# Performance work log

Hardware: AMD Instinct MI355X
Metric: run time of the kernel (lower is better)

Reference implementation:

```python
import jax, jax.numpy as jnp
import numpy as np

EPS = 1e-5
BLOCKS = 8

def _bn(x, g, b, m, v):
    # eval-mode BatchNorm1d over channel dim of [B, C, T]
    return g[:, None] * (x - m[:, None]) * jax.lax.rsqrt(v[:, None] + EPS) + b[:, None]

def _conv1x1(x, w):
    # x: [B, Cin, T], w: [Cout, Cin] -> [B, Cout, T]
    return jnp.einsum('bct,oc->bot', x, w)

def _dwconv(x, w, dil):
    # x: [B, C, T], w: [C, K] depthwise dilated conv, 'same' padding
    C, K = w.shape
    pad = dil * (K - 1) // 2
    return jax.lax.conv_general_dilated(
        x, w[:, None, :], window_strides=(1,), padding=[(pad, pad)],
        rhs_dilation=(dil,), dimension_numbers=('NCH', 'OIH', 'NCH'),
        feature_group_count=C)

def setup_inputs() -> dict:
    key = jax.random.key(0)
    ks = jax.random.split(key, 16)
    B, Cb, H, T, K = 16, 256, 512, 4096, 3
    d = {}
    d['x'] = jax.random.normal(ks[0], (B, Cb, T), jnp.float32)
    d['bn1_gamma'] = jax.random.uniform(ks[1], (BLOCKS, Cb), jnp.float32)
    d['bn1_beta'] = jax.random.normal(ks[2], (BLOCKS, Cb), jnp.float32)
    d['bn1_mean'] = jax.random.normal(ks[3], (BLOCKS, Cb), jnp.float32)
    d['bn1_var'] = jax.random.uniform(ks[4], (BLOCKS, Cb), jnp.float32)
    d['w1'] = jax.random.normal(ks[5], (BLOCKS, H, Cb), jnp.float32)
    d['bn2_gamma'] = jax.random.uniform(ks[6], (BLOCKS, H), jnp.float32)
    d['bn2_beta'] = jax.random.normal(ks[7], (BLOCKS, H), jnp.float32)
    d['bn2_mean'] = jax.random.normal(ks[8], (BLOCKS, H), jnp.float32)
    d['bn2_var'] = jax.random.uniform(ks[9], (BLOCKS, H), jnp.float32)
    d['dw_w'] = jax.random.normal(ks[10], (BLOCKS, H, K), jnp.float32)
    d['bn3_gamma'] = jax.random.uniform(ks[11], (BLOCKS, H), jnp.float32)
    d['bn3_beta'] = jax.random.normal(ks[12], (BLOCKS, H), jnp.float32)
    d['bn3_mean'] = jax.random.normal(ks[13], (BLOCKS, H), jnp.float32)
    d['bn3_var'] = jax.random.uniform(ks[14], (BLOCKS, H), jnp.float32)
    d['w2'] = jax.random.normal(ks[15], (BLOCKS, Cb, H), jnp.float32)
    return d

def reference(x, bn1_gamma, bn1_beta, bn1_mean, bn1_var, w1,
              bn2_gamma, bn2_beta, bn2_mean, bn2_var, dw_w,
              bn3_gamma, bn3_beta, bn3_mean, bn3_var, w2):
    sign = jnp.sign  # binary activation on inputs and weights
    resid = x
    for i in range(BLOCKS):
        dil = 2 ** i
        h = _bn(resid, bn1_gamma[i], bn1_beta[i], bn1_mean[i], bn1_var[i])
        h = _conv1x1(sign(h), sign(w1[i]))                 # 1x1, Cb -> H
        h = _bn(h, bn2_gamma[i], bn2_beta[i], bn2_mean[i], bn2_var[i])
        h = _dwconv(sign(h), sign(dw_w[i]), dil)           # depthwise dilated
        h = _bn(h, bn3_gamma[i], bn3_beta[i], bn3_mean[i], bn3_var[i])
        h = _conv1x1(sign(h), sign(w2[i]))                 # 1x1, H -> Cb
        resid = resid + h
    return resid
```

## Files before the change

### kernel.cpp

```cpp
#include <hip/hip_runtime.h>
#include <stdint.h>

namespace {
constexpr int Bn  = 16;
constexpr int Cc  = 256;
constexpr int Hn  = 512;
constexpr int Tn  = 4096;
constexpr int CWn = Cc / 32;
constexpr int HWn = Hn / 32;
constexpr int TWn = Tn / 32;
constexpr int TC  = 64;
constexpr float EPSf = 1e-5f;
}

__global__ __launch_bounds__(256) void setup_kernel(
    const float* __restrict__ bn1g, const float* __restrict__ bn1b,
    const float* __restrict__ bn1m, const float* __restrict__ bn1v,
    const float* __restrict__ w1,
    const float* __restrict__ bn2g, const float* __restrict__ bn2b,
    const float* __restrict__ bn2m, const float* __restrict__ bn2v,
    const float* __restrict__ dww,
    const float* __restrict__ bn3g, const float* __restrict__ bn3b,
    const float* __restrict__ bn3m, const float* __restrict__ bn3v,
    const float* __restrict__ w2,
    float* __restrict__ thr1, float* __restrict__ thr2, float* __restrict__ thr3,
    uint32_t* __restrict__ dws, uint32_t* __restrict__ W1p, uint32_t* __restrict__ W2p)
{
  const int idx = blockIdx.x * 256 + threadIdx.x;
  if (idx < 8 * Hn * CWn) {
    const int w = idx & (CWn - 1);
    const int h = idx >> 3;
    const float* src = w1 + (size_t)h * Cc + w * 32;
    uint32_t word = 0;
#pragma unroll
    for (int j = 0; j < 32; ++j) word |= (uint32_t)(src[j] > 0.f) << j;
    W1p[h * CWn + w] = word;
  } else {
    const int k = idx - 8 * Hn * CWn;
    const int w = k & (HWn - 1);
    const int c = k >> 4;
    const float* src = w2 + (size_t)c * Hn + w * 32;
    uint32_t word = 0;
#pragma unroll
    for (int j = 0; j < 32; ++j) word |= (uint32_t)(src[j] > 0.f) << j;
    W2p[c * HWn + w] = word;
  }
  if (idx < 8 * Cc)
    thr1[idx] = bn1m[idx] - bn1b[idx] * sqrtf(bn1v[idx] + EPSf) / bn1g[idx];
  if (idx < 8 * Hn) {
    thr2[idx] = bn2m[idx] - bn2b[idx] * sqrtf(bn2v[idx] + EPSf) / bn2g[idx];
    thr3[idx] = bn3m[idx] - bn3b[idx] * sqrtf(bn3v[idx] + EPSf) / bn3g[idx];
    uint32_t dw = 0;
    for (int k = 0; k < 3; ++k) dw |= (uint32_t)(dww[(size_t)idx * 3 + k] > 0.f) << k;
    dws[idx] = dw;
  }
}

__global__ __launch_bounds__(256) void k1_pack(
    const float* __restrict__ resid, const float* __restrict__ thr1,
    uint32_t* __restrict__ Xp)
{
  const int idx = blockIdx.x * 256 + threadIdx.x;
  const int t  = idx & (Tn - 1);
  const int cw = (idx >> 12) & (CWn - 1);
  const int b  = idx >> 15;
  const float* r = resid + ((size_t)(b * Cc + cw * 32)) * Tn + t;
  uint32_t word = 0;
#pragma unroll
  for (int j = 0; j < 32; ++j)
    word |= (uint32_t)(r[(size_t)j * Tn] > thr1[cw * 32 + j]) << j;
  Xp[((size_t)b * CWn + cw) * Tn + t] = word;
}

__global__ __launch_bounds__(256) void k2_gemm1(
    const uint32_t* __restrict__ Xp, const uint32_t* __restrict__ W1p,
    const float* __restrict__ thr2, uint32_t* __restrict__ Y)
{
  const int bid  = blockIdx.x;
  const int tblk = bid & 15;
  const int og   = (bid >> 4) & 63;
  const int b    = bid >> 10;
  const int t    = tblk * 256 + threadIdx.x;
  const int o    = og * 8;

  const uint32_t* xrow = Xp + (size_t)b * CWn * Tn + t;
  const uint32_t* wrow = W1p + o * CWn;
  int acc[8] = {0, 0, 0, 0, 0, 0, 0, 0};
#pragma unroll
  for (int w = 0; w < CWn; ++w) {
    const uint32_t xw = xrow[(size_t)w * Tn];
#pragma unroll
    for (int r = 0; r < 8; ++r)
      acc[r] += __popc(xw ^ wrow[r * CWn + w]);
  }
  const int lane = threadIdx.x & 63;
#pragma unroll
  for (int r = 0; r < 8; ++r) {
    const float v = (float)(Cc - 2 * acc[r]);
    const uint64_t m = __ballot(v > thr2[o + r]);
    if ((lane & 31) == 0)
      Y[((size_t)b * TWn + (t >> 5)) * Hn + o + r] = (uint32_t)(m >> lane);
  }
}

__global__ __launch_bounds__(512) void k_iter(
    const uint32_t* __restrict__ Yin, const uint32_t* __restrict__ dws,
    const float* __restrict__ thr3, const uint32_t* __restrict__ W2p,
    const float* __restrict__ rin, float* __restrict__ rout,
    const float* __restrict__ thr1n, const uint32_t* __restrict__ W1n,
    const float* __restrict__ thr2n, uint32_t* __restrict__ Yout,
    int dil, int do_next)
{
  __shared__ uint32_t Zlds[HWn * TC];
  __shared__ uint32_t Xlds[CWn * TC];

  const int chunk = blockIdx.x & (Tn / TC - 1);
  const int b     = blockIdx.x >> 6;
  const int lane  = threadIdx.x & 63;
  const int wid   = __builtin_amdgcn_readfirstlane(threadIdx.x >> 6);
  const int lh    = lane & 31;
  const int twL   = lane >> 5;
  const int tw0   = chunk * 2;

#pragma unroll
  for (int task = 0; task < 2; ++task) {
    const int hw = wid * 2 + task;
    const int tw = tw0 + twL;
    const int ch = hw * 32 + lh;

    const uint32_t* yb = Yin + (size_t)b * TWn * Hn + ch;
    const uint32_t ycur = yb[(size_t)tw * Hn];
    uint32_t yl, yr, Vl, Vr;
    if (dil >= 32) {
      const int dw = dil >> 5;
      const bool lok = tw >= dw, rok = tw + dw < TWn;
      yl = lok ? yb[(size_t)(tw - dw) * Hn] : 0u;
      yr = rok ? yb[(size_t)(tw + dw) * Hn] : 0u;
      Vl = lok ? ~0u : 0u;
      Vr = rok ? ~0u : 0u;
    } else {
      const uint32_t yp = (tw > 0) ? yb[(size_t)(tw - 1) * Hn] : 0u;
      const uint32_t yn = (tw < TWn - 1) ? yb[(size_t)(tw + 1) * Hn] : 0u;
      yl = (ycur << dil) | ((tw > 0) ? (yp >> (32 - dil)) : 0u);
      yr = (ycur >> dil) | ((tw < TWn - 1) ? (yn << (32 - dil)) : 0u);
      Vl = (tw == 0) ? (~0u << dil) : ~0u;
      Vr = (tw == TWn - 1) ? (~0u >> dil) : ~0u;
    }
    const uint32_t d = dws[ch];
    const uint32_t a  = ((d & 1u) ? yl : ~yl) & Vl;
    const uint32_t bb = (d & 2u) ? ycur : ~ycur;
    const uint32_t c  = ((d & 4u) ? yr : ~yr) & Vr;

    const float thr = thr3[ch];
    const float v3 = (thr + 3.f) * 0.5f;
    const float v2 = (thr + 2.f) * 0.5f;
    const int K3 = (int)(v3 >= 0.f) + (int)(v3 >= 1.f) + (int)(v3 >= 2.f) + (int)(v3 >= 3.f);
    const int K2 = (int)(v2 >= 0.f) + (int)(v2 >= 1.f) + (int)(v2 >= 2.f);

    const uint32_t g1 = a | bb | c;
    const uint32_t g2 = (a & bb) | (c & (a | bb));
    const uint32_t g3 = a & bb & c;
    const uint32_t full = (K3 == 0) ? ~0u : (K3 == 1) ? g1 : (K3 == 2) ? g2
                        : (K3 == 3) ? g3 : 0u;
    const uint32_t lm = (K2 == 0) ? ~0u : (K2 == 1) ? (bb | c) : (K2 == 2) ? (bb & c) : 0u;
    const uint32_t rm = (K2 == 0) ? ~0u : (K2 == 1) ? (a | bb) : (K2 == 2) ? (a & bb) : 0u;

    uint32_t w = (Vl & Vr & full) | (~Vl & lm) | (~Vr & rm);

#pragma unroll
    for (int s = 16; s; s >>= 1) {
      const uint32_t m = 0xFFFFFFFFu / ((1u << s) + 1u);
      const uint32_t o = __shfl_xor(w, s, 64);
      w = ((lane & s) == 0) ? ((w & m) | ((o & m) << s))
                            : ((w & ~m) | ((o & ~m) >> s));
    }
    Zlds[hw * TC + twL * 32 + lh] = w;
  }
  __syncthreads();

  {
    const int cw = wid;
    const int tl = lane;
    const int tg = chunk * TC + tl;

    uint32_t z[HWn];
#pragma unroll
    for (int w = 0; w < HWn; ++w) z[w] = Zlds[w * TC + tl];

    const uint32_t* wrow = W2p + (cw * 32) * HWn;
    const size_t base = ((size_t)(b * Cc + cw * 32)) * Tn + tg;
    const float* rp = rin + base;
    float* op = rout + base;
    uint32_t word = 0;
#pragma unroll 1
    for (int jo = 0; jo < 32; jo += 8) {
      float rv[8];
#pragma unroll
      for (int jj = 0; jj < 8; ++jj)
        rv[jj] = rp[(size_t)(jo + jj) * Tn];
#pragma unroll
      for (int jj = 0; jj < 8; ++jj) {
        const int j = jo + jj;
        int acc = 0;
#pragma unroll
        for (int w = 0; w < HWn; ++w) acc += __popc(z[w] ^ wrow[j * HWn + w]);
        const float ro = rv[jj] + (float)(Hn - 2 * acc);
        op[(size_t)j * Tn] = ro;
        word |= (uint32_t)(ro > thr1n[cw * 32 + j]) << j;
      }
    }
    Xlds[cw * TC + tl] = word;
  }
  __syncthreads();

  if (do_next) {
    const int t  = chunk * TC + lane;
    uint32_t x[CWn];
#pragma unroll
    for (int w = 0; w < CWn; ++w) x[w] = Xlds[w * TC + lane];

    uint32_t* yo = Yout + ((size_t)b * TWn + (t >> 5)) * Hn;
#pragma unroll 1
    for (int r = 0; r < 8; ++r) {
      const int o = wid * 64 + r * 8;
      const uint32_t* wrow = W1n + o * CWn;
      int acc[8] = {0, 0, 0, 0, 0, 0, 0, 0};
#pragma unroll
      for (int w = 0; w < CWn; ++w) {
        const uint32_t xw = x[w];
#pragma unroll
        for (int q = 0; q < 8; ++q)
          acc[q] += __popc(xw ^ wrow[q * CWn + w]);
      }
#pragma unroll
      for (int q = 0; q < 8; ++q) {
        const float v = (float)(Cc - 2 * acc[q]);
        const uint64_t m = __ballot(v > thr2n[o + q]);
        if ((lane & 31) == 0)
          yo[o + q] = (uint32_t)(m >> lane);
      }
    }
  }
}

extern "C" void kernel_launch(void* const* d_in, const int* in_sizes, int n_in,
                              void* d_out, int out_size, void* d_ws, size_t ws_size,
                              hipStream_t stream)
{
  const float* x     = (const float*)d_in[0];
  const float* bn1g  = (const float*)d_in[1];
  const float* bn1b  = (const float*)d_in[2];
  const float* bn1m  = (const float*)d_in[3];
  const float* bn1v  = (const float*)d_in[4];
  const float* w1    = (const float*)d_in[5];
  const float* bn2g  = (const float*)d_in[6];
  const float* bn2b  = (const float*)d_in[7];
  const float* bn2m  = (const float*)d_in[8];
  const float* bn2v  = (const float*)d_in[9];
  const float* dww   = (const float*)d_in[10];
  const float* bn3g  = (const float*)d_in[11];
  const float* bn3b  = (const float*)d_in[12];
  const float* bn3m  = (const float*)d_in[13];
  const float* bn3v  = (const float*)d_in[14];
  const float* w2    = (const float*)d_in[15];
  float* out = (float*)d_out;

  char* ws = (char*)d_ws;
  uint32_t* Xp  = (uint32_t*)(ws);
  uint32_t* Ya  = (uint32_t*)(ws + (2u  << 20));
  uint32_t* Yb  = (uint32_t*)(ws + (6u  << 20));
  uint32_t* W1p = (uint32_t*)(ws + (10u << 20));
  uint32_t* W2p = (uint32_t*)(ws + (10u << 20) + (128u << 10));
  float*    thr1 = (float*)(ws + (10u << 20) + (256u << 10));
  float*    thr2 = thr1 + 8 * Cc;
  float*    thr3 = thr2 + 8 * Hn;
  uint32_t* dws  = (uint32_t*)(thr3 + 8 * Hn);

  setup_kernel<<<256, 256, 0, stream>>>(bn1g, bn1b, bn1m, bn1v, w1,
                                        bn2g, bn2b, bn2m, bn2v, dww,
                                        bn3g, bn3b, bn3m, bn3v, w2,
                                        thr1, thr2, thr3, dws, W1p, W2p);

  k1_pack <<<2048,  256, 0, stream>>>(x, thr1, Xp);
  k2_gemm1<<<16384, 256, 0, stream>>>(Xp, W1p, thr2, Ya);

  for (int i = 0; i < 8; ++i) {
    const float* rin = (i == 0) ? x : out;
    const int inext = (i < 7) ? i + 1 : 7;
    const uint32_t* Yin  = (i & 1) ? Yb : Ya;
    uint32_t*       Yout = (i & 1) ? Ya : Yb;
    k_iter<<<1024, 512, 0, stream>>>(Yin, dws + i * Hn, thr3 + i * Hn,
                                     W2p + i * Cc * HWn, rin, out,
                                     thr1 + inext * Cc, W1p + inext * Hn * CWn,
                                     thr2 + inext * Hn, Yout,
                                     1 << i, (i < 7) ? 1 : 0);
  }
}
```

Measured before the change: 437.6 us.

## Compute next-block binary GEMM1 with int8 MFMA instead of XOR-popcount

Result: faster. 382.2 us (-12.7%).

```diff
diff --git a/kernel.cpp b/kernel.cpp
--- a/kernel.cpp
+++ b/kernel.cpp
@@ -12,6 +12,9 @@
 constexpr int TC  = 64;
 constexpr float EPSf = 1e-5f;
 }
+
+typedef __attribute__((ext_vector_type(4)))  int i32x4;
+typedef __attribute__((ext_vector_type(16))) int i32x16;
 
 __global__ __launch_bounds__(256) void setup_kernel(
     const float* __restrict__ bn1g, const float* __restrict__ bn1b,
@@ -24,7 +27,8 @@
     const float* __restrict__ bn3m, const float* __restrict__ bn3v,
     const float* __restrict__ w2,
     float* __restrict__ thr1, float* __restrict__ thr2, float* __restrict__ thr3,
-    uint32_t* __restrict__ dws, uint32_t* __restrict__ W1p, uint32_t* __restrict__ W2p)
+    uint32_t* __restrict__ dws, uint32_t* __restrict__ W1p, uint32_t* __restrict__ W2p,
+    uint8_t* __restrict__ W1u, int* __restrict__ Sw1, int* __restrict__ T2i)
 {
   const int idx = blockIdx.x * 256 + threadIdx.x;
   if (idx < 8 * Hn * CWn) {
@@ -35,6 +39,14 @@
 #pragma unroll
     for (int j = 0; j < 32; ++j) word |= (uint32_t)(src[j] > 0.f) << j;
     W1p[h * CWn + w] = word;
+    atomicAdd(&Sw1[h], (int)__popc(word));
+    uint32_t* dst = (uint32_t*)(W1u + (size_t)h * 256);
+#pragma unroll
+    for (int q = 0; q < 8; ++q) {
+      const uint32_t dw = (((word >> (4 * q)) & 0xFu) * 0x00204081u) & 0x01010101u;
+      const int off = (w * 32 + q * 4) ^ ((h & 15) << 4);
+      dst[off >> 2] = dw;
+    }
   } else {
     const int k = idx - 8 * Hn * CWn;
     const int w = k & (HWn - 1);
@@ -48,10 +60,17 @@
   if (idx < 8 * Cc)
     thr1[idx] = bn1m[idx] - bn1b[idx] * sqrtf(bn1v[idx] + EPSf) / bn1g[idx];
   if (idx < 8 * Hn) {
-    thr2[idx] = bn2m[idx] - bn2b[idx] * sqrtf(bn2v[idx] + EPSf) / bn2g[idx];
+    const float th2 = bn2m[idx] - bn2b[idx] * sqrtf(bn2v[idx] + EPSf) / bn2g[idx];
+    thr2[idx] = th2;
+    int T;
+    if (th2 >= 8.0e6f)       T =  (1 << 24);
+    else if (th2 <= -8.0e6f) T = -(1 << 24);
+    else if (th2 == th2)     T = (int)floorf(th2) + 1;
+    else                     T =  (1 << 24);
+    T2i[idx] = T;
     thr3[idx] = bn3m[idx] - bn3b[idx] * sqrtf(bn3v[idx] + EPSf) / bn3g[idx];
     uint32_t dw = 0;
-    for (int k = 0; k < 3; ++k) dw |= (uint32_t)(dww[(size_t)idx * 3 + k] > 0.f) << k;
+    for (int k2 = 0; k2 < 3; ++k2) dw |= (uint32_t)(dww[(size_t)idx * 3 + k2] > 0.f) << k2;
     dws[idx] = dw;
   }
 }
@@ -107,20 +126,27 @@
     const uint32_t* __restrict__ Yin, const uint32_t* __restrict__ dws,
     const float* __restrict__ thr3, const uint32_t* __restrict__ W2p,
     const float* __restrict__ rin, float* __restrict__ rout,
-    const float* __restrict__ thr1n, const uint32_t* __restrict__ W1n,
-    const float* __restrict__ thr2n, uint32_t* __restrict__ Yout,
+    const float* __restrict__ thr1n,
+    const uint8_t* __restrict__ W1u_n, const int* __restrict__ Sw1_n,
+    const int* __restrict__ T2i_n, uint32_t* __restrict__ Yout,
     int dil, int do_next)
 {
   __shared__ uint32_t Zlds[HWn * TC];
-  __shared__ uint32_t Xlds[CWn * TC];
+  __shared__ __align__(16) uint8_t Xi8[TC * 256];
+  __shared__ __align__(16) uint8_t Wbuf[128 * 256];
+  __shared__ int Sx[TC];
+  __shared__ int Tc[Hn];
 
   const int chunk = blockIdx.x & (Tn / TC - 1);
   const int b     = blockIdx.x >> 6;
-  const int lane  = threadIdx.x & 63;
-  const int wid   = __builtin_amdgcn_readfirstlane(threadIdx.x >> 6);
+  const int tid   = threadIdx.x;
+  const int lane  = tid & 63;
+  const int wid   = __builtin_amdgcn_readfirstlane(tid >> 6);
   const int lh    = lane & 31;
   const int twL   = lane >> 5;
   const int tw0   = chunk * 2;
+
+  if (tid < TC) Sx[tid] = 0;
 
 #pragma unroll
   for (int task = 0; task < 2; ++task) {
@@ -191,6 +217,7 @@
     const size_t base = ((size_t)(b * Cc + cw * 32)) * Tn + tg;
     const float* rp = rin + base;
     float* op = rout + base;
+    const int swz = (tl & 15) << 4;
     uint32_t word = 0;
 #pragma unroll 1
     for (int jo = 0; jo < 32; jo += 8) {
@@ -198,6 +225,7 @@
 #pragma unroll
       for (int jj = 0; jj < 8; ++jj)
         rv[jj] = rp[(size_t)(jo + jj) * Tn];
+      uint32_t blo = 0, bhi = 0;
 #pragma unroll
       for (int jj = 0; jj < 8; ++jj) {
         const int j = jo + jj;
@@ -206,39 +234,67 @@
         for (int w = 0; w < HWn; ++w) acc += __popc(z[w] ^ wrow[j * HWn + w]);
         const float ro = rv[jj] + (float)(Hn - 2 * acc);
         op[(size_t)j * Tn] = ro;
-        word |= (uint32_t)(ro > thr1n[cw * 32 + j]) << j;
+        const uint32_t bit = (uint32_t)(ro > thr1n[cw * 32 + j]);
+        word |= bit << j;
+        if (jj < 4) blo |= bit << (jj * 8);
+        else        bhi |= bit << ((jj - 4) * 8);
       }
-    }
-    Xlds[cw * TC + tl] = word;
+      const int c0 = cw * 32 + jo;
+      *(uint32_t*)&Xi8[tl * 256 + (c0 ^ swz)]     = blo;
+      *(uint32_t*)&Xi8[tl * 256 + (c0 ^ swz) + 4] = bhi;
+    }
+    atomicAdd(&Sx[tl], (int)__popc(word));
   }
   __syncthreads();
 
   if (do_next) {
-    const int t  = chunk * TC + lane;
-    uint32_t x[CWn];
-#pragma unroll
-    for (int w = 0; w < CWn; ++w) x[w] = Xlds[w * TC + lane];
-
-    uint32_t* yo = Yout + ((size_t)b * TWn + (t >> 5)) * Hn;
+    Tc[tid] = T2i_n[tid] + 2 * Sw1_n[tid] - 256;
+
+    const int ntile = wid & 1;
+    const int mloc  = wid >> 1;
+    const int tloc  = ntile * 32 + (lane & 31);
+    const int half  = lane >> 5;
+
+    i32x4 bf[8];
+#pragma unroll
+    for (int ks = 0; ks < 8; ++ks) {
+      const int koff = (ks * 32 + half * 16) ^ ((tloc & 15) << 4);
+      bf[ks] = *(const i32x4*)&Xi8[tloc * 256 + koff];
+    }
+    const int Sxv2 = 2 * Sx[tloc];
+    uint32_t* yo = Yout + ((size_t)b * TWn + (chunk * 2 + ntile)) * Hn;
+
 #pragma unroll 1
-    for (int r = 0; r < 8; ++r) {
-      const int o = wid * 64 + r * 8;
-      const uint32_t* wrow = W1n + o * CWn;
-      int acc[8] = {0, 0, 0, 0, 0, 0, 0, 0};
-#pragma unroll
-      for (int w = 0; w < CWn; ++w) {
-        const uint32_t xw = x[w];
-#pragma unroll
-        for (int q = 0; q < 8; ++q)
-          acc[q] += __popc(xw ^ wrow[q * CWn + w]);
+    for (int msup = 0; msup < 4; ++msup) {
+      const uint32_t* gsrc = (const uint32_t*)(W1u_n + msup * 32768);
+      uint32_t* ldst = (uint32_t*)Wbuf;
+      i32x4 stg[4];
+#pragma unroll
+      for (int s = 0; s < 4; ++s)
+        stg[s] = *(const i32x4*)&gsrc[(s * 512 + tid) * 4];
+#pragma unroll
+      for (int s = 0; s < 4; ++s)
+        *(i32x4*)&ldst[(s * 512 + tid) * 4] = stg[s];
+      __syncthreads();
+
+      const int lrow = mloc * 32 + (lane & 31);
+      i32x16 acc = {0,0,0,0, 0,0,0,0, 0,0,0,0, 0,0,0,0};
+#pragma unroll
+      for (int ks = 0; ks < 8; ++ks) {
+        const int aoff = (ks * 32 + half * 16) ^ ((lrow & 15) << 4);
+        const i32x4 af = *(const i32x4*)&Wbuf[lrow * 256 + aoff];
+        acc = __builtin_amdgcn_mfma_i32_32x32x32_i8(af, bf[ks], acc, 0, 0, 0);
       }
-#pragma unroll
-      for (int q = 0; q < 8; ++q) {
-        const float v = (float)(Cc - 2 * acc[q]);
-        const uint64_t m = __ballot(v > thr2n[o + q]);
-        if ((lane & 31) == 0)
-          yo[o + q] = (uint32_t)(m >> lane);
+
+      const int obase = msup * 128 + mloc * 32;
+#pragma unroll
+      for (int r = 0; r < 16; ++r) {
+        const int row = (r & 3) + 8 * (r >> 2) + 4 * half;
+        const int o = obase + row;
+        const uint64_t m = __ballot((acc[r] << 2) >= Tc[o] + Sxv2);
+        if ((lane & 31) == 0) yo[o] = (uint32_t)(m >> lane);
       }
+      __syncthreads();
     }
   }
 }
@@ -275,11 +331,17 @@
   float*    thr2 = thr1 + 8 * Cc;
   float*    thr3 = thr2 + 8 * Hn;
   uint32_t* dws  = (uint32_t*)(thr3 + 8 * Hn);
+  uint8_t*  W1u  = (uint8_t*)(ws + (11u << 20));
+  int*      Sw1  = (int*)(ws + (12u << 20));
+  int*      T2i  = (int*)(ws + (12u << 20) + (16u << 10));
+
+  hipMemsetAsync(Sw1, 0, 8 * Hn * sizeof(int), stream);
 
   setup_kernel<<<256, 256, 0, stream>>>(bn1g, bn1b, bn1m, bn1v, w1,
                                         bn2g, bn2b, bn2m, bn2v, dww,
                                         bn3g, bn3b, bn3m, bn3v, w2,
-                                        thr1, thr2, thr3, dws, W1p, W2p);
+                                        thr1, thr2, thr3, dws, W1p, W2p,
+                                        W1u, Sw1, T2i);
 
   k1_pack <<<2048,  256, 0, stream>>>(x, thr1, Xp);
   k2_gemm1<<<16384, 256, 0, stream>>>(Xp, W1p, thr2, Ya);
@@ -291,8 +353,9 @@
     uint32_t*       Yout = (i & 1) ? Ya : Yb;
     k_iter<<<1024, 512, 0, stream>>>(Yin, dws + i * Hn, thr3 + i * Hn,
                                      W2p + i * Cc * HWn, rin, out,
-                                     thr1 + inext * Cc, W1p + inext * Hn * CWn,
-                                     thr2 + inext * Hn, Yout,
-                                     1 << i, (i < 7) ? 1 : 0);
-  }
-}
+                                     thr1 + inext * Cc,
+                                     W1u + (size_t)inext * Hn * 256,
+                                     Sw1 + inext * Hn, T2i + inext * Hn,
+                                     Yout, 1 << i, (i < 7) ? 1 : 0);
+  }
+}
```
